# Optimization experiments

Hardware: AMD Instinct MI355X
Metric: run time of the kernel (lower is better)

The kernel has to match this reference:

```python
import jax, jax.numpy as jnp
import numpy as np

B, S, I, H = 32, 1024, 1024, 1024

def setup_inputs() -> dict:
    key = jax.random.key(0)
    k1, k2, k3, k4, k5 = jax.random.split(key, 5)
    bound = 1.0 / np.sqrt(I + H)  # nn.Linear default init scale
    return {
        "x": jax.random.normal(k1, (B, S, I), dtype=jnp.float32),
        "h0": jax.random.normal(k2, (1, B, H), dtype=jnp.float32),
        "c0": jax.random.normal(k3, (1, B, H), dtype=jnp.float32),
        "W": jax.random.uniform(k4, (H, I + H), dtype=jnp.float32, minval=-bound, maxval=bound),
        "b": jax.random.uniform(k5, (H,), dtype=jnp.float32, minval=-bound, maxval=bound),
    }

def reference(x, h0, c0, W, b):
    # NOTE: original torch module applies the SAME linear layer to h_x for all
    # four gates, so f_t == i_t == o_t == sigmoid(z) and C_tilde = tanh(z).
    # Concat order is (h, x): W[:, :H] multiplies h, W[:, H:] multiplies x.
    Wh = W[:, :x.shape[-1] if False else h0.shape[-1]]  # [H, H]
    Wx = W[:, h0.shape[-1]:]                            # [H, I]
    h_init = h0[0]  # [B, H]
    c_init = c0[0]  # [B, H]
    # Precompute the input contribution for all timesteps in one big GEMM.
    xz = jnp.einsum('bsi,hi->sbh', x, Wx) + b  # [S, B, H]

    def step(carry, xz_t):
        h, c = carry
        z = h @ Wh.T + xz_t          # [B, H] shared gate pre-activation
        s = jax.nn.sigmoid(z)        # f_t == i_t == o_t
        c_new = s * c + s * jnp.tanh(z)
        h_new = s * jnp.tanh(c_new)
        return (h_new, c_new), h_new

    (hn, cn), outs = jax.lax.scan(step, (h_init, c_init), xz)
    out = jnp.swapaxes(outs, 0, 1)  # [B, S, H]
    return out, hn[None], cn[None]
```

## Files before the change

### kernel.cpp

```cpp
#include <hip/hip_runtime.h>

#define B_ 32
#define S_ 1024
#define H_ 1024
#define NWG 64
#define EXN (32 * 1024)

typedef float f32x4 __attribute__((ext_vector_type(4)));
typedef short bf16x8 __attribute__((ext_vector_type(8)));
typedef unsigned int u32x4 __attribute__((ext_vector_type(4)));
typedef unsigned short u16;

__device__ __forceinline__ short f2bf(float f) {
  union { float f; unsigned u; } v; v.f = f;
  unsigned r = v.u + 0x7FFFu + ((v.u >> 16) & 1u);
  return (short)(r >> 16);
}

__global__ __launch_bounds__(256) void xz_gemm(
    const float* __restrict__ X, const float* __restrict__ W,
    const float* __restrict__ bias, float* __restrict__ C) {
  __shared__ short As[128][40];
  __shared__ short Bs[128][40];
  const int tid  = threadIdx.x;
  const int lane = tid & 63, wave = tid >> 6;
  const int m0 = blockIdx.y * 128, n0 = blockIdx.x * 128;
  const int wm = (wave >> 1) * 64, wn = (wave & 1) * 64;
  const int jl = lane & 15, kq = lane >> 4;
  const int sr = tid >> 2, skg = (tid & 3) * 8;

  f32x4 zero4 = {0.f, 0.f, 0.f, 0.f};
  f32x4 acc[4][4];
  #pragma unroll
  for (int mi = 0; mi < 4; ++mi)
    #pragma unroll
    for (int ni = 0; ni < 4; ++ni) acc[mi][ni] = zero4;

  for (int k0 = 0; k0 < 1024; k0 += 32) {
    #pragma unroll
    for (int rr = 0; rr < 2; ++rr) {
      int row = sr + rr * 64;
      const float* pa = X + (size_t)(m0 + row) * 1024 + k0 + skg;
      f32x4 a0 = *(const f32x4*)pa;
      f32x4 a1 = *(const f32x4*)(pa + 4);
      bf16x8 pk;
      #pragma unroll
      for (int e = 0; e < 4; ++e) { pk[e] = f2bf(a0[e]); pk[e + 4] = f2bf(a1[e]); }
      *(bf16x8*)&As[row][skg] = pk;
      const float* pb = W + (size_t)(n0 + row) * 2048 + 1024 + k0 + skg;
      f32x4 b0 = *(const f32x4*)pb;
      f32x4 b1 = *(const f32x4*)(pb + 4);
      bf16x8 qk;
      #pragma unroll
      for (int e = 0; e < 4; ++e) { qk[e] = f2bf(b0[e]); qk[e + 4] = f2bf(b1[e]); }
      *(bf16x8*)&Bs[row][skg] = qk;
    }
    __syncthreads();
    bf16x8 af[4], bfv[4];
    #pragma unroll
    for (int mi = 0; mi < 4; ++mi) af[mi] = *(const bf16x8*)&As[wm + mi * 16 + jl][kq * 8];
    #pragma unroll
    for (int ni = 0; ni < 4; ++ni) bfv[ni] = *(const bf16x8*)&Bs[wn + ni * 16 + jl][kq * 8];
    #pragma unroll
    for (int mi = 0; mi < 4; ++mi)
      #pragma unroll
      for (int ni = 0; ni < 4; ++ni)
        acc[mi][ni] = __builtin_amdgcn_mfma_f32_16x16x32_bf16(af[mi], bfv[ni], acc[mi][ni], 0, 0, 0);
    __syncthreads();
  }
  #pragma unroll
  for (int ni = 0; ni < 4; ++ni) {
    int col = n0 + wn + ni * 16 + jl;
    float bv = bias[col];
    #pragma unroll
    for (int mi = 0; mi < 4; ++mi) {
      int rbase = m0 + wm + mi * 16 + kq * 4;
      #pragma unroll
      for (int r = 0; r < 4; ++r)
        C[(size_t)(rbase + r) * 1024 + col] = acc[mi][ni][r] + bv;
    }
  }
}

__global__ __launch_bounds__(512) void lstm_rec(
    const float* __restrict__ W, const float* __restrict__ h0,
    const float* __restrict__ c0, float* __restrict__ out,
    u16* __restrict__ exch) {
  __shared__ float zred[2][8][2][64][5];
  const int tid  = threadIdx.x;
  const int lane = tid & 63, wave = tid >> 6;
  const int jl = lane & 15, kq = lane >> 4;
  const int bg = blockIdx.x >> 5;
  const int cg = blockIdx.x & 31;

  const int bp  = tid >> 5;
  const int cp  = tid & 31;
  const int b   = bg * 16 + bp;
  const int col = cg * 32 + cp;
  float cst  = c0[b * 1024 + col];
  float hcur = h0[b * 1024 + col];

#define PUBLISH(HVAL, VER) do {                                               \
    unsigned hb = (unsigned)(u16)f2bf(HVAL);                                  \
    if ((cp & 7) == 7) hb = (hb & 0xFFFEu) | (((unsigned)(VER) >> 1) & 1u);   \
    unsigned ot = (unsigned)__shfl_xor((int)hb, 1);                           \
    unsigned v0 = (lane & 1) ? (ot | (hb << 16)) : (hb | (ot << 16));         \
    unsigned o2 = (unsigned)__shfl_xor((int)v0, 2);                           \
    unsigned w0 = (lane & 2) ? o2 : v0;                                       \
    unsigned w1 = (lane & 2) ? v0 : o2;                                       \
    unsigned o0 = (unsigned)__shfl_xor((int)w0, 4);                           \
    unsigned o1 = (unsigned)__shfl_xor((int)w1, 4);                           \
    u32x4 g;                                                                  \
    g[0] = (lane & 4) ? o0 : w0;  g[1] = (lane & 4) ? o1 : w1;                \
    g[2] = (lane & 4) ? w0 : o0;  g[3] = (lane & 4) ? w1 : o1;                \
    if ((lane & 7) == 0) {                                                    \
      u16* dp = exch + (size_t)((VER) & 1) * EXN + b * 1024 + (col & ~7);     \
      asm volatile("global_store_dwordx4 %0, %1, off sc0 sc1"                 \
                   :: "v"(dp), "v"(g) : "memory");                            \
    }                                                                         \
  } while (0)

  PUBLISH(hcur, 0);

  bf16x8 bfr[2][4];
  #pragma unroll
  for (int ct = 0; ct < 2; ++ct)
    #pragma unroll
    for (int kk = 0; kk < 4; ++kk) {
      const float* pw = W + (size_t)(cg * 32 + ct * 16 + jl) * 2048
                          + wave * 128 + kk * 32 + kq * 8;
      f32x4 a0 = *(const f32x4*)pw;
      f32x4 a1 = *(const f32x4*)(pw + 4);
      bf16x8 pk;
      #pragma unroll
      for (int e = 0; e < 4; ++e) { pk[e] = f2bf(a0[e]); pk[e + 4] = f2bf(a1[e]); }
      bfr[ct][kk] = pk;
    }

  const int ct_o = cp >> 4;
  const int lred = ((bp >> 2) << 4) | (cp & 15);
  const int rred = bp & 3;
  const size_t obase = (size_t)b * (S_ * H_) + col;
  const u16* aB = exch + (size_t)(bg * 16 + jl) * 1024 + wave * 128 + kq * 8;

  asm volatile("s_waitcnt vmcnt(0)" ::: "memory");
  float xz = out[obase];

  for (int t = 0; t < S_; ++t) {
    const int p = t & 1;
    const unsigned etg = (unsigned)((t >> 1) & 1);
    const u16* src = aB + (size_t)p * EXN;

    u32x4 L0, L1, L2, L3;
    int spin = 0;
    for (;;) {
      asm volatile("global_load_dwordx4 %0, %1, off sc0 sc1"
                   : "=v"(L0) : "v"(src) : "memory");
      asm volatile("global_load_dwordx4 %0, %1, off offset:64 sc0 sc1"
                   : "=v"(L1) : "v"(src) : "memory");
      asm volatile("global_load_dwordx4 %0, %1, off offset:128 sc0 sc1"
                   : "=v"(L2) : "v"(src) : "memory");
      asm volatile("global_load_dwordx4 %0, %1, off offset:192 sc0 sc1"
                   : "=v"(L3) : "v"(src) : "memory");
      asm volatile("s_waitcnt vmcnt(0)" ::: "memory");
      __builtin_amdgcn_sched_barrier(0);
      unsigned bad = ((L0[3] >> 16) ^ etg) | ((L1[3] >> 16) ^ etg)
                   | ((L2[3] >> 16) ^ etg) | ((L3[3] >> 16) ^ etg);
      if (__all((bad & 1u) == 0u)) break;
      if (++spin >= 16384) break;
      if (spin > 256) __builtin_amdgcn_s_sleep(2);
    }

    union { u32x4 u; bf16x8 h; } q0, q1, q2, q3;
    q0.u = L0; q1.u = L1; q2.u = L2; q3.u = L3;
    bf16x8 afr[4] = {q0.h, q1.h, q2.h, q3.h};
    #pragma unroll
    for (int ct = 0; ct < 2; ++ct) {
      f32x4 pacc = {0.f, 0.f, 0.f, 0.f};
      #pragma unroll
      for (int kk = 0; kk < 4; ++kk)
        pacc = __builtin_amdgcn_mfma_f32_16x16x32_bf16(afr[kk], bfr[ct][kk], pacc, 0, 0, 0);
      #pragma unroll
      for (int r = 0; r < 4; ++r)
        zred[p][wave][ct][lane][r] = pacc[r];
    }

    __syncthreads();

    float z = xz;
    #pragma unroll
    for (int w = 0; w < 8; ++w) z += zred[p][w][ct_o][lred][rred];
    float u  = __expf(-z);
    float u2 = u * u;
    float sg = __builtin_amdgcn_rcpf(1.f + u);
    float tz = (1.f - u2) * __builtin_amdgcn_rcpf(1.f + u2);
    cst  = sg * (cst + tz);
    float v  = __expf(-2.f * cst);
    float tc = (1.f - v) * __builtin_amdgcn_rcpf(1.f + v);
    hcur = sg * tc;

    PUBLISH(hcur, t + 1);
    out[obase + (size_t)t * H_] = hcur;
    asm volatile("s_waitcnt vmcnt(0)" ::: "memory");
    xz = out[obase + (size_t)(t + 1 < S_ ? t + 1 : t) * H_];
  }
#undef PUBLISH

  const size_t OFS = (size_t)B_ * S_ * H_;
  out[OFS + b * 1024 + col] = hcur;
  out[OFS + (size_t)B_ * H_ + b * 1024 + col] = cst;
}

extern "C" void kernel_launch(void* const* d_in, const int* in_sizes, int n_in,
                              void* d_out, int out_size, void* d_ws, size_t ws_size,
                              hipStream_t stream) {
  const float* x    = (const float*)d_in[0];
  const float* h0   = (const float*)d_in[1];
  const float* c0   = (const float*)d_in[2];
  const float* W    = (const float*)d_in[3];
  const float* bias = (const float*)d_in[4];
  float* out = (float*)d_out;

  u16* exch = (u16*)d_ws;
  hipMemsetAsync(exch, 0xFF, 2 * EXN * sizeof(u16), stream);

  xz_gemm<<<dim3(8, 256), 256, 0, stream>>>(x, W, bias, out);
  lstm_rec<<<dim3(NWG), 512, 0, stream>>>(W, h0, c0, out, exch);
}
```

Measured before the change: 2.351 ms.

## Fuse input GEMM into recurrent kernel and overlap via per-chunk counters

Merges the xz GEMM and the recurrent LSTM kernel into one launch. The first 64 blocks run the recurrence while the remaining 2048 blocks compute the input projection in 128-timestep chunks, publishing completion through atomic counters. The recurrence waits on a counter only at chunk boundaries, so most of the GEMM runs concurrently with the serial scan instead of before it. The 512-thread blocks leave half the waves idle during GEMM MFMA work, and correctness depends on the 64 recurrent blocks being resident alongside the GEMM blocks. A per-step s_sleep is also added to the recurrent loop.

```diff
diff --git a/kernel.cpp b/kernel.cpp
--- a/kernel.cpp
+++ b/kernel.cpp
@@ -3,7 +3,8 @@
 #define B_ 32
 #define S_ 1024
 #define H_ 1024
-#define NWG 64
+#define NWG_REC 64
+#define NWG_GEMM 2048
 #define EXN (32 * 1024)
 
 typedef float f32x4 __attribute__((ext_vector_type(4)));
@@ -16,83 +17,99 @@
   unsigned r = v.u + 0x7FFFu + ((v.u >> 16) & 1u);
   return (short)(r >> 16);
 }
-
-__global__ __launch_bounds__(256) void xz_gemm(
+__device__ __forceinline__ float ldg_coh_f32(const float* p) {
+  float r;
+  asm volatile("global_load_dword %0, %1, off sc0 sc1" : "=v"(r) : "v"(p) : "memory");
+  return r;
+}
+__device__ __forceinline__ void stg_coh_f32(float* p, float v) {
+  asm volatile("global_store_dword %0, %1, off sc0 sc1" :: "v"(p), "v"(v) : "memory");
+}
+
+__global__ __launch_bounds__(512) void lstm_fused(
     const float* __restrict__ X, const float* __restrict__ W,
-    const float* __restrict__ bias, float* __restrict__ C) {
-  __shared__ short As[128][40];
-  __shared__ short Bs[128][40];
-  const int tid  = threadIdx.x;
-  const int lane = tid & 63, wave = tid >> 6;
-  const int m0 = blockIdx.y * 128, n0 = blockIdx.x * 128;
-  const int wm = (wave >> 1) * 64, wn = (wave & 1) * 64;
-  const int jl = lane & 15, kq = lane >> 4;
-  const int sr = tid >> 2, skg = (tid & 3) * 8;
-
-  f32x4 zero4 = {0.f, 0.f, 0.f, 0.f};
-  f32x4 acc[4][4];
-  #pragma unroll
-  for (int mi = 0; mi < 4; ++mi)
-    #pragma unroll
-    for (int ni = 0; ni < 4; ++ni) acc[mi][ni] = zero4;
-
-  for (int k0 = 0; k0 < 1024; k0 += 32) {
-    #pragma unroll
-    for (int rr = 0; rr < 2; ++rr) {
-      int row = sr + rr * 64;
-      const float* pa = X + (size_t)(m0 + row) * 1024 + k0 + skg;
-      f32x4 a0 = *(const f32x4*)pa;
-      f32x4 a1 = *(const f32x4*)(pa + 4);
-      bf16x8 pk;
-      #pragma unroll
-      for (int e = 0; e < 4; ++e) { pk[e] = f2bf(a0[e]); pk[e + 4] = f2bf(a1[e]); }
-      *(bf16x8*)&As[row][skg] = pk;
-      const float* pb = W + (size_t)(n0 + row) * 2048 + 1024 + k0 + skg;
-      f32x4 b0 = *(const f32x4*)pb;
-      f32x4 b1 = *(const f32x4*)(pb + 4);
-      bf16x8 qk;
-      #pragma unroll
-      for (int e = 0; e < 4; ++e) { qk[e] = f2bf(b0[e]); qk[e + 4] = f2bf(b1[e]); }
-      *(bf16x8*)&Bs[row][skg] = qk;
-    }
-    __syncthreads();
-    bf16x8 af[4], bfv[4];
-    #pragma unroll
-    for (int mi = 0; mi < 4; ++mi) af[mi] = *(const bf16x8*)&As[wm + mi * 16 + jl][kq * 8];
-    #pragma unroll
-    for (int ni = 0; ni < 4; ++ni) bfv[ni] = *(const bf16x8*)&Bs[wn + ni * 16 + jl][kq * 8];
-    #pragma unroll
-    for (int mi = 0; mi < 4; ++mi)
-      #pragma unroll
-      for (int ni = 0; ni < 4; ++ni)
-        acc[mi][ni] = __builtin_amdgcn_mfma_f32_16x16x32_bf16(af[mi], bfv[ni], acc[mi][ni], 0, 0, 0);
-    __syncthreads();
-  }
-  #pragma unroll
-  for (int ni = 0; ni < 4; ++ni) {
-    int col = n0 + wn + ni * 16 + jl;
-    float bv = bias[col];
-    #pragma unroll
-    for (int mi = 0; mi < 4; ++mi) {
-      int rbase = m0 + wm + mi * 16 + kq * 4;
-      #pragma unroll
-      for (int r = 0; r < 4; ++r)
-        C[(size_t)(rbase + r) * 1024 + col] = acc[mi][ni][r] + bv;
-    }
-  }
-}
-
-__global__ __launch_bounds__(512) void lstm_rec(
-    const float* __restrict__ W, const float* __restrict__ h0,
+    const float* __restrict__ bias, const float* __restrict__ h0,
     const float* __restrict__ c0, float* __restrict__ out,
-    u16* __restrict__ exch) {
-  __shared__ float zred[2][8][2][64][5];
+    u16* __restrict__ exch, unsigned* __restrict__ cnt) {
+  __shared__ union {
+    float zred[2][8][2][64][5];
+    struct { short As[128][40]; short Bs[128][40]; } g;
+  } sm;
   const int tid  = threadIdx.x;
   const int lane = tid & 63, wave = tid >> 6;
   const int jl = lane & 15, kq = lane >> 4;
+
+  if (blockIdx.x >= NWG_REC) {
+    const int g    = blockIdx.x - NWG_REC;
+    const int sblk = g >> 8;
+    const int b    = (g & 255) >> 3;
+    const int n    = g & 7;
+    const int m0 = b * 1024 + sblk * 128, n0 = n * 128;
+    const int wm = (wave >> 1) * 64, wn = (wave & 1) * 64;
+    const int sr = tid >> 2, skg = (tid & 3) * 8;
+
+    f32x4 acc[4][4];
+    #pragma unroll
+    for (int mi = 0; mi < 4; ++mi)
+      #pragma unroll
+      for (int ni = 0; ni < 4; ++ni) acc[mi][ni] = (f32x4){0.f, 0.f, 0.f, 0.f};
+
+    for (int k0 = 0; k0 < 1024; k0 += 32) {
+      {
+        const float* pa = X + (size_t)(m0 + sr) * 1024 + k0 + skg;
+        f32x4 a0 = *(const f32x4*)pa;
+        f32x4 a1 = *(const f32x4*)(pa + 4);
+        bf16x8 pk;
+        #pragma unroll
+        for (int e = 0; e < 4; ++e) { pk[e] = f2bf(a0[e]); pk[e + 4] = f2bf(a1[e]); }
+        *(bf16x8*)&sm.g.As[sr][skg] = pk;
+        const float* pb = W + (size_t)(n0 + sr) * 2048 + 1024 + k0 + skg;
+        f32x4 b0 = *(const f32x4*)pb;
+        f32x4 b1 = *(const f32x4*)(pb + 4);
+        bf16x8 qk;
+        #pragma unroll
+        for (int e = 0; e < 4; ++e) { qk[e] = f2bf(b0[e]); qk[e + 4] = f2bf(b1[e]); }
+        *(bf16x8*)&sm.g.Bs[sr][skg] = qk;
+      }
+      __syncthreads();
+      if (wave < 4) {
+        bf16x8 af[4], bfv[4];
+        #pragma unroll
+        for (int mi = 0; mi < 4; ++mi) af[mi] = *(const bf16x8*)&sm.g.As[wm + mi * 16 + jl][kq * 8];
+        #pragma unroll
+        for (int ni = 0; ni < 4; ++ni) bfv[ni] = *(const bf16x8*)&sm.g.Bs[wn + ni * 16 + jl][kq * 8];
+        #pragma unroll
+        for (int mi = 0; mi < 4; ++mi)
+          #pragma unroll
+          for (int ni = 0; ni < 4; ++ni)
+            acc[mi][ni] = __builtin_amdgcn_mfma_f32_16x16x32_bf16(af[mi], bfv[ni], acc[mi][ni], 0, 0, 0);
+      }
+      __syncthreads();
+    }
+    if (wave < 4) {
+      #pragma unroll
+      for (int ni = 0; ni < 4; ++ni) {
+        int colc = n0 + wn + ni * 16 + jl;
+        float bv = bias[colc];
+        #pragma unroll
+        for (int mi = 0; mi < 4; ++mi) {
+          int rbase = m0 + wm + mi * 16 + kq * 4;
+          #pragma unroll
+          for (int r = 0; r < 4; ++r)
+            stg_coh_f32(out + (size_t)(rbase + r) * 1024 + colc, acc[mi][ni][r] + bv);
+        }
+      }
+    }
+    asm volatile("s_waitcnt vmcnt(0)" ::: "memory");
+    __syncthreads();
+    if (tid == 0)
+      __hip_atomic_fetch_add(&cnt[sblk], 1u, __ATOMIC_RELAXED,
+                             __HIP_MEMORY_SCOPE_AGENT);
+    return;
+  }
+
   const int bg = blockIdx.x >> 5;
   const int cg = blockIdx.x & 31;
-
   const int bp  = tid >> 5;
   const int cp  = tid & 31;
   const int b   = bg * 16 + bp;
@@ -110,13 +127,13 @@
     unsigned w1 = (lane & 2) ? v0 : o2;                                       \
     unsigned o0 = (unsigned)__shfl_xor((int)w0, 4);                           \
     unsigned o1 = (unsigned)__shfl_xor((int)w1, 4);                           \
-    u32x4 g;                                                                  \
-    g[0] = (lane & 4) ? o0 : w0;  g[1] = (lane & 4) ? o1 : w1;                \
-    g[2] = (lane & 4) ? w0 : o0;  g[3] = (lane & 4) ? w1 : o1;                \
+    u32x4 gg;                                                                 \
+    gg[0] = (lane & 4) ? o0 : w0;  gg[1] = (lane & 4) ? o1 : w1;              \
+    gg[2] = (lane & 4) ? w0 : o0;  gg[3] = (lane & 4) ? w1 : o1;              \
     if ((lane & 7) == 0) {                                                    \
       u16* dp = exch + (size_t)((VER) & 1) * EXN + b * 1024 + (col & ~7);     \
       asm volatile("global_store_dwordx4 %0, %1, off sc0 sc1"                 \
-                   :: "v"(dp), "v"(g) : "memory");                            \
+                   :: "v"(dp), "v"(gg) : "memory");                           \
     }                                                                         \
   } while (0)
 
@@ -143,8 +160,10 @@
   const size_t obase = (size_t)b * (S_ * H_) + col;
   const u16* aB = exch + (size_t)(bg * 16 + jl) * 1024 + wave * 128 + kq * 8;
 
-  asm volatile("s_waitcnt vmcnt(0)" ::: "memory");
-  float xz = out[obase];
+  while (__hip_atomic_load(&cnt[0], __ATOMIC_RELAXED, __HIP_MEMORY_SCOPE_AGENT)
+         < 256u)
+    __builtin_amdgcn_s_sleep(16);
+  float xz = ldg_coh_f32(out + obase);
 
   for (int t = 0; t < S_; ++t) {
     const int p = t & 1;
@@ -182,14 +201,14 @@
         pacc = __builtin_amdgcn_mfma_f32_16x16x32_bf16(afr[kk], bfr[ct][kk], pacc, 0, 0, 0);
       #pragma unroll
       for (int r = 0; r < 4; ++r)
-        zred[p][wave][ct][lane][r] = pacc[r];
+        sm.zred[p][wave][ct][lane][r] = pacc[r];
     }
 
     __syncthreads();
 
     float z = xz;
     #pragma unroll
-    for (int w = 0; w < 8; ++w) z += zred[p][w][ct_o][lred][rred];
+    for (int w = 0; w < 8; ++w) z += sm.zred[p][w][ct_o][lred][rred];
     float u  = __expf(-z);
     float u2 = u * u;
     float sg = __builtin_amdgcn_rcpf(1.f + u);
@@ -201,8 +220,18 @@
 
     PUBLISH(hcur, t + 1);
     out[obase + (size_t)t * H_] = hcur;
-    asm volatile("s_waitcnt vmcnt(0)" ::: "memory");
-    xz = out[obase + (size_t)(t + 1 < S_ ? t + 1 : t) * H_];
+
+    if (t + 1 < S_) {
+      if (((t + 1) & 127) == 0) {
+        const unsigned* cb = &cnt[(t + 1) >> 7];
+        while (__hip_atomic_load(cb, __ATOMIC_RELAXED, __HIP_MEMORY_SCOPE_AGENT)
+               < 256u)
+          __builtin_amdgcn_s_sleep(16);
+      }
+      xz = ldg_coh_f32(out + obase + (size_t)(t + 1) * H_);
+    }
+
+    __builtin_amdgcn_s_sleep(8);
   }
 #undef PUBLISH
 
@@ -222,8 +251,10 @@
   float* out = (float*)d_out;
 
   u16* exch = (u16*)d_ws;
+  unsigned* cnt = (unsigned*)((char*)d_ws + 2 * EXN * sizeof(u16));
   hipMemsetAsync(exch, 0xFF, 2 * EXN * sizeof(u16), stream);
-
-  xz_gemm<<<dim3(8, 256), 256, 0, stream>>>(x, W, bias, out);
-  lstm_rec<<<dim3(NWG), 512, 0, stream>>>(W, h0, c0, out, exch);
-}
+  hipMemsetAsync(cnt, 0, 8 * sizeof(unsigned), stream);
+
+  lstm_fused<<<dim3(NWG_REC + NWG_GEMM), 512, 0, stream>>>(
+      x, W, bias, h0, c0, out, exch, cnt);
+}
```

After: 2.448 ms. 4.2% more time.
